# Optimization experiments

Measured on AMD Instinct MI355X. Metric: run time of the kernel, lower is better.

The kernel has to match this reference:

```python
import jax, jax.numpy as jnp
import numpy as np

M, K, N = 8192, 4096, 4096  # tokens, in_features, out_features


def setup_inputs() -> dict:
    key = jax.random.key(0)
    k1, k2, k3, k4, k5, k6 = jax.random.split(key, 6)
    return {
        "x_q": jax.random.randint(k1, (M, K), 0, 256, dtype=jnp.int32),
        "weight_int8": jax.random.randint(k2, (N, K), 0, 256, dtype=jnp.int32),
        "weight_scale": jax.random.uniform(k3, (N, 1), dtype=jnp.float32) * 0.01 + 1e-4,
        "weight_zero_point": jax.random.randint(k4, (N, 1), 0, 256, dtype=jnp.int32),
        "bias": jax.random.normal(k5, (N,), dtype=jnp.float32),
        "input_scale": jax.random.uniform(k6, (1,), dtype=jnp.float32) * 0.05 + 1e-4,
        "input_zero_point": 128,
    }


def reference(x_q, weight_int8, weight_scale, weight_zero_point, bias, input_scale, input_zero_point):
    # zero-point-subtracted fp32 operands (simulated int32 accumulation in fp32)
    x_f = x_q.astype(jnp.float32) - jnp.float32(input_zero_point)      # [M, K]
    w_f = weight_int8.astype(jnp.float32) - weight_zero_point.astype(jnp.float32)  # [N, K]
    acc = jnp.einsum('mk,nk->mn', x_f, w_f)                            # [M, N]
    dequant_scale = input_scale * weight_scale.T                       # [1, N]
    return acc * dequant_scale + bias                                  # [M, N]
```

## Files before the change

### kernel.cpp

```cpp
#include <hip/hip_runtime.h>
#include <hip/hip_bf16.h>
#include <stdint.h>

typedef int v4i __attribute__((ext_vector_type(4)));

#define AS_GLOBAL(p) ((const __attribute__((address_space(1))) void*)(p))
#define AS_LDS(p)    ((__attribute__((address_space(3))) void*)(p))

__global__ __launch_bounds__(256) void prep_kernel(const int* __restrict__ x,
                                                   const int* __restrict__ w,
                                                   const int* __restrict__ izp_p,
                                                   signed char* __restrict__ xs,
                                                   signed char* __restrict__ wsq,
                                                   int* __restrict__ rowsum, int M, int K) {
    int row = blockIdx.x;
    int n4 = K >> 2;
    if (row < M) {
        int izp = izp_p[0];
        const int4* xr = (const int4*)(x + (long)row * K);
        uint32_t* xo = (uint32_t*)(xs + (long)row * K);
        int sum = 0;
        for (int i = threadIdx.x; i < n4; i += 256) {
            int4 v = xr[i];
            int a0 = v.x - izp, a1 = v.y - izp, a2 = v.z - izp, a3 = v.w - izp;
            sum += a0 + a1 + a2 + a3;
            xo[i] = (uint32_t)(a0 & 0xFF) | ((uint32_t)(a1 & 0xFF) << 8) |
                    ((uint32_t)(a2 & 0xFF) << 16) | ((uint32_t)(a3 & 0xFF) << 24);
        }
        sum += __shfl_down(sum, 32);
        sum += __shfl_down(sum, 16);
        sum += __shfl_down(sum, 8);
        sum += __shfl_down(sum, 4);
        sum += __shfl_down(sum, 2);
        sum += __shfl_down(sum, 1);
        __shared__ int red[4];
        if ((threadIdx.x & 63) == 0) red[threadIdx.x >> 6] = sum;
        __syncthreads();
        if (threadIdx.x == 0) rowsum[row] = red[0] + red[1] + red[2] + red[3];
    } else {
        int wrow = row - M;
        const int4* wr = (const int4*)(w + (long)wrow * K);
        uint32_t* wo = (uint32_t*)(wsq + (long)wrow * K);
        for (int i = threadIdx.x; i < n4; i += 256) {
            int4 v = wr[i];
            int a0 = v.x - 128, a1 = v.y - 128, a2 = v.z - 128, a3 = v.w - 128;
            wo[i] = (uint32_t)(a0 & 0xFF) | ((uint32_t)(a1 & 0xFF) << 8) |
                    ((uint32_t)(a2 & 0xFF) << 16) | ((uint32_t)(a3 & 0xFF) << 24);
        }
    }
}


#define BAR  __builtin_amdgcn_s_barrier()
#define LGKM0 asm volatile("s_waitcnt lgkmcnt(0)" ::: "memory")
#define VM8  asm volatile("s_waitcnt vmcnt(8)" ::: "memory")
#define VM0  asm volatile("s_waitcnt vmcnt(0)" ::: "memory")
#define PRIO1 __builtin_amdgcn_s_setprio(1)
#define PRIO0 __builtin_amdgcn_s_setprio(0)

#define STAGE(bb, tile) do {                                                          \
    int t_ = (tile); if (t_ >= NT) t_ = NT - 1;                                       \
    long ko_ = (long)t_ * 64;                                                         \
    signed char* lb_ = lds + (bb) * 32768 + w * 2048;                                 \
    __builtin_amdgcn_global_load_lds(AS_GLOBAL(gA0 + ko_), AS_LDS(lb_),         16, 0, 0); \
    __builtin_amdgcn_global_load_lds(AS_GLOBAL(gA1 + ko_), AS_LDS(lb_ + 1024),  16, 0, 0); \
    __builtin_amdgcn_global_load_lds(AS_GLOBAL(gB0 + ko_), AS_LDS(lb_ + 16384), 16, 0, 0); \
    __builtin_amdgcn_global_load_lds(AS_GLOBAL(gB1 + ko_), AS_LDS(lb_ + 17408), 16, 0, 0); \
  } while (0)

#define M1(mi, ni)                                                                     \
    acc[mi][ni] = __builtin_amdgcn_mfma_i32_16x16x64_i8(af[mi], bf[ni], acc[mi][ni], 0, 0, 0);

__global__ __launch_bounds__(512, 2) void gemm_i8_p4(
    const signed char* __restrict__ A,
    const signed char* __restrict__ B,
    const int* __restrict__ rowsum, const float* __restrict__ wscale,
    const int* __restrict__ wzp, const float* __restrict__ bias,
    const float* __restrict__ iscale, float* __restrict__ C,
    int M, int N, int K) {
  __shared__ signed char lds[131072];
  const int tid = threadIdx.x;
  const int w = tid >> 6, l = tid & 63;
  const int wm = w >> 2, wn = w & 3;
  const int fr = l & 15, fq = l >> 4;

  int nwg = gridDim.x, bid = blockIdx.x;
  if ((nwg & 7) == 0) { int cpx = nwg >> 3; bid = (bid & 7) * cpx + (bid >> 3); }
  const int ntiles = N >> 8;
  const int mt = bid / ntiles, nt = bid - mt * ntiles;
  const long brow = (long)mt << 8, bcol = (long)nt << 8;

  const int NT = K >> 6;

  const int sr = l >> 2;
  const int schunk = ((l & 3) ^ ((l >> 3) & 3)) << 4;
  const signed char* gA0 = A + (brow + (w * 2 + 0) * 16 + sr) * (long)K + schunk;
  const signed char* gA1 = A + (brow + (w * 2 + 1) * 16 + sr) * (long)K + schunk;
  const signed char* gB0 = B + (bcol + (w * 2 + 0) * 16 + sr) * (long)K + schunk;
  const signed char* gB1 = B + (bcol + (w * 2 + 1) * 16 + sr) * (long)K + schunk;

  const int rdc = (fq ^ ((fr >> 1) & 3)) << 4;
  const int aoffc = (wm * 128 + fr) * 64 + rdc;
  const int boffc = 16384 + (wn * 64 + fr) * 64 + rdc;

  v4i acc[8][4] = {};
  v4i af[8], bf[4];

  STAGE(0, 0); STAGE(1, 1); STAGE(2, 2);
  VM8; BAR;

  for (int t = 0; t < NT; ++t) {
    const int bufo = (t & 3) << 15;
#pragma unroll
    for (int mi = 0; mi < 8; ++mi) af[mi] = *(const v4i*)(lds + bufo + aoffc + mi * 1024);
#pragma unroll
    for (int ni = 0; ni < 4; ++ni) bf[ni] = *(const v4i*)(lds + bufo + boffc + ni * 1024);
    STAGE((t + 3) & 3, t + 3);
    PRIO1;
    M1(0, 0) M1(0, 1) M1(0, 2) M1(0, 3)
    M1(1, 0) M1(1, 1) M1(1, 2) M1(1, 3)
    M1(2, 0) M1(2, 1) M1(2, 2) M1(2, 3)
    M1(3, 0) M1(3, 1) M1(3, 2) M1(3, 3)
    M1(4, 0) M1(4, 1) M1(4, 2) M1(4, 3)
    M1(5, 0) M1(5, 1) M1(5, 2) M1(5, 3)
    M1(6, 0) M1(6, 1) M1(6, 2) M1(6, 3)
    M1(7, 0) M1(7, 1) M1(7, 2) M1(7, 3)
    PRIO0;
    LGKM0;
    VM8;
    BAR;
  }

  const float is = iscale[0];
  int rs[8][4];
#pragma unroll
  for (int mi = 0; mi < 8; ++mi)
#pragma unroll
    for (int j = 0; j < 4; ++j)
      rs[mi][j] = rowsum[(int)brow + wm * 128 + mi * 16 + fq * 4 + j];
#pragma unroll
  for (int ni = 0; ni < 4; ++ni) {
    const int col = (int)bcol + wn * 64 + ni * 16 + fr;
    const float sc = is * wscale[col];
    const int zpc = 128 - wzp[col];
    const float bi = bias[col];
#pragma unroll
    for (int mi = 0; mi < 8; ++mi) {
      const int row0 = (int)brow + wm * 128 + mi * 16 + fq * 4;
#pragma unroll
      for (int j = 0; j < 4; ++j) {
        const int v = acc[mi][ni][j] + zpc * rs[mi][j];
        C[(long)(row0 + j) * N + col] = (float)v * sc + bi;
      }
    }
  }
}

extern "C" void kernel_launch(void* const* d_in, const int* in_sizes, int n_in,
                              void* d_out, int out_size, void* d_ws, size_t ws_size,
                              hipStream_t stream) {
    const int* x_q = (const int*)d_in[0];
    const int* w_q = (const int*)d_in[1];
    const float* wscale = (const float*)d_in[2];
    const int* wzp = (const int*)d_in[3];
    const float* bias = (const float*)d_in[4];
    const float* iscale = (const float*)d_in[5];
    const int* izp = (const int*)d_in[6];

    int N = in_sizes[2];
    int K = in_sizes[1] / N;
    int M = in_sizes[0] / K;

    signed char* xs = (signed char*)d_ws;
    signed char* wsq = xs + (size_t)M * K;
    int* rowsum = (int*)(wsq + (size_t)N * K);

    prep_kernel<<<M + N, 256, 0, stream>>>(x_q, w_q, izp, xs, wsq, rowsum, M, K);

    int grid = (M / 256) * (N / 256);
    gemm_i8_p4<<<grid, 512, 0, stream>>>(xs, wsq, rowsum, wscale, wzp, bias, iscale,
                                         (float*)d_out, M, N, K);
}
```

Measured before the change: 192.0 us.

## Load B fragments directly to registers and shrink A LDS staging to double buffer

B operand fragments are now loaded from global memory straight into registers with register double-buffering, while only A is staged through LDS using two 16KB buffers instead of a four-deep 128KB ring. This cuts LDS footprint so more workgroups can reside per CU and removes LDS writes/reads for B. In exchange, the pipeline depth drops to one tile ahead with a full vmcnt(0) wait each iteration, and B global reads are duplicated across waves sharing columns and less coalesced.

Result: slower. 262.9 us (+36.9%).

```diff
diff --git a/kernel.cpp b/kernel.cpp
--- a/kernel.cpp
+++ b/kernel.cpp
@@ -53,32 +53,59 @@
 
 #define BAR  __builtin_amdgcn_s_barrier()
 #define LGKM0 asm volatile("s_waitcnt lgkmcnt(0)" ::: "memory")
-#define VM8  asm volatile("s_waitcnt vmcnt(8)" ::: "memory")
 #define VM0  asm volatile("s_waitcnt vmcnt(0)" ::: "memory")
 #define PRIO1 __builtin_amdgcn_s_setprio(1)
 #define PRIO0 __builtin_amdgcn_s_setprio(0)
 
-#define STAGE(bb, tile) do {                                                          \
-    int t_ = (tile); if (t_ >= NT) t_ = NT - 1;                                       \
-    long ko_ = (long)t_ * 64;                                                         \
-    signed char* lb_ = lds + (bb) * 32768 + w * 2048;                                 \
-    __builtin_amdgcn_global_load_lds(AS_GLOBAL(gA0 + ko_), AS_LDS(lb_),         16, 0, 0); \
-    __builtin_amdgcn_global_load_lds(AS_GLOBAL(gA1 + ko_), AS_LDS(lb_ + 1024),  16, 0, 0); \
-    __builtin_amdgcn_global_load_lds(AS_GLOBAL(gB0 + ko_), AS_LDS(lb_ + 16384), 16, 0, 0); \
-    __builtin_amdgcn_global_load_lds(AS_GLOBAL(gB1 + ko_), AS_LDS(lb_ + 17408), 16, 0, 0); \
+#define STAGE_A(bb, tile) do {                                                        \
+    long ko_ = (long)(tile) * 64;                                                     \
+    signed char* lb_ = lds + (bb) * 16384 + w * 2048;                                 \
+    __builtin_amdgcn_global_load_lds(AS_GLOBAL(gA0 + ko_), AS_LDS(lb_),        16, 0, 0); \
+    __builtin_amdgcn_global_load_lds(AS_GLOBAL(gA1 + ko_), AS_LDS(lb_ + 1024), 16, 0, 0); \
   } while (0)
 
-#define M1(mi, ni)                                                                     \
-    acc[mi][ni] = __builtin_amdgcn_mfma_i32_16x16x64_i8(af[mi], bf[ni], acc[mi][ni], 0, 0, 0);
-
-__global__ __launch_bounds__(512, 2) void gemm_i8_p4(
+#define M1(mi, ni, BC)                                                                 \
+    acc[mi][ni] = __builtin_amdgcn_mfma_i32_16x16x64_i8(af[mi], BC[ni], acc[mi][ni], 0, 0, 0);
+
+#define MFMA32(BC) do {                                                                \
+    M1(0, 0, BC) M1(0, 1, BC) M1(0, 2, BC) M1(0, 3, BC)                                \
+    M1(1, 0, BC) M1(1, 1, BC) M1(1, 2, BC) M1(1, 3, BC)                                \
+    M1(2, 0, BC) M1(2, 1, BC) M1(2, 2, BC) M1(2, 3, BC)                                \
+    M1(3, 0, BC) M1(3, 1, BC) M1(3, 2, BC) M1(3, 3, BC)                                \
+    M1(4, 0, BC) M1(4, 1, BC) M1(4, 2, BC) M1(4, 3, BC)                                \
+    M1(5, 0, BC) M1(5, 1, BC) M1(5, 2, BC) M1(5, 3, BC)                                \
+    M1(6, 0, BC) M1(6, 1, BC) M1(6, 2, BC) M1(6, 3, BC)                                \
+    M1(7, 0, BC) M1(7, 1, BC) M1(7, 2, BC) M1(7, 3, BC)                                \
+  } while (0)
+
+#define ITER(b, BC, BN, t) do {                                                        \
+    int tn_ = (t) + 1; if (tn_ >= NT) tn_ = NT - 1;                                    \
+    long bo_ = (long)tn_ * 64;                                                         \
+    BN[0] = *(const v4i*)(gBf0 + bo_);                                                 \
+    BN[1] = *(const v4i*)(gBf1 + bo_);                                                 \
+    BN[2] = *(const v4i*)(gBf2 + bo_);                                                 \
+    BN[3] = *(const v4i*)(gBf3 + bo_);                                                 \
+    STAGE_A((b) ^ 1, tn_);                                                             \
+    af[0] = *(const v4i*)(lds + (b) * 16384 + aoffc + 0 * 1024);                       \
+    af[1] = *(const v4i*)(lds + (b) * 16384 + aoffc + 1 * 1024);                       \
+    af[2] = *(const v4i*)(lds + (b) * 16384 + aoffc + 2 * 1024);                       \
+    af[3] = *(const v4i*)(lds + (b) * 16384 + aoffc + 3 * 1024);                       \
+    af[4] = *(const v4i*)(lds + (b) * 16384 + aoffc + 4 * 1024);                       \
+    af[5] = *(const v4i*)(lds + (b) * 16384 + aoffc + 5 * 1024);                       \
+    af[6] = *(const v4i*)(lds + (b) * 16384 + aoffc + 6 * 1024);                       \
+    af[7] = *(const v4i*)(lds + (b) * 16384 + aoffc + 7 * 1024);                       \
+    PRIO1; MFMA32(BC); PRIO0;                                                          \
+    LGKM0; VM0; BAR;                                                                   \
+  } while (0)
+
+__global__ __launch_bounds__(512, 2) void gemm_i8_bd(
     const signed char* __restrict__ A,
     const signed char* __restrict__ B,
     const int* __restrict__ rowsum, const float* __restrict__ wscale,
     const int* __restrict__ wzp, const float* __restrict__ bias,
     const float* __restrict__ iscale, float* __restrict__ C,
     int M, int N, int K) {
-  __shared__ signed char lds[131072];
+  __shared__ signed char lds[32768];
   const int tid = threadIdx.x;
   const int w = tid >> 6, l = tid & 63;
   const int wm = w >> 2, wn = w & 3;
@@ -96,39 +123,29 @@
   const int schunk = ((l & 3) ^ ((l >> 3) & 3)) << 4;
   const signed char* gA0 = A + (brow + (w * 2 + 0) * 16 + sr) * (long)K + schunk;
   const signed char* gA1 = A + (brow + (w * 2 + 1) * 16 + sr) * (long)K + schunk;
-  const signed char* gB0 = B + (bcol + (w * 2 + 0) * 16 + sr) * (long)K + schunk;
-  const signed char* gB1 = B + (bcol + (w * 2 + 1) * 16 + sr) * (long)K + schunk;
 
   const int rdc = (fq ^ ((fr >> 1) & 3)) << 4;
   const int aoffc = (wm * 128 + fr) * 64 + rdc;
-  const int boffc = 16384 + (wn * 64 + fr) * 64 + rdc;
+
+  const signed char* gBf0 = B + (bcol + wn * 64 + 0 * 16 + fr) * (long)K + fq * 16;
+  const signed char* gBf1 = B + (bcol + wn * 64 + 1 * 16 + fr) * (long)K + fq * 16;
+  const signed char* gBf2 = B + (bcol + wn * 64 + 2 * 16 + fr) * (long)K + fq * 16;
+  const signed char* gBf3 = B + (bcol + wn * 64 + 3 * 16 + fr) * (long)K + fq * 16;
 
   v4i acc[8][4] = {};
-  v4i af[8], bf[4];
-
-  STAGE(0, 0); STAGE(1, 1); STAGE(2, 2);
-  VM8; BAR;
-
-  for (int t = 0; t < NT; ++t) {
-    const int bufo = (t & 3) << 15;
-#pragma unroll
-    for (int mi = 0; mi < 8; ++mi) af[mi] = *(const v4i*)(lds + bufo + aoffc + mi * 1024);
-#pragma unroll
-    for (int ni = 0; ni < 4; ++ni) bf[ni] = *(const v4i*)(lds + bufo + boffc + ni * 1024);
-    STAGE((t + 3) & 3, t + 3);
-    PRIO1;
-    M1(0, 0) M1(0, 1) M1(0, 2) M1(0, 3)
-    M1(1, 0) M1(1, 1) M1(1, 2) M1(1, 3)
-    M1(2, 0) M1(2, 1) M1(2, 2) M1(2, 3)
-    M1(3, 0) M1(3, 1) M1(3, 2) M1(3, 3)
-    M1(4, 0) M1(4, 1) M1(4, 2) M1(4, 3)
-    M1(5, 0) M1(5, 1) M1(5, 2) M1(5, 3)
-    M1(6, 0) M1(6, 1) M1(6, 2) M1(6, 3)
-    M1(7, 0) M1(7, 1) M1(7, 2) M1(7, 3)
-    PRIO0;
-    LGKM0;
-    VM8;
-    BAR;
+  v4i af[8];
+  v4i bfA[4], bfB[4];
+
+  STAGE_A(0, 0);
+  bfA[0] = *(const v4i*)(gBf0);
+  bfA[1] = *(const v4i*)(gBf1);
+  bfA[2] = *(const v4i*)(gBf2);
+  bfA[3] = *(const v4i*)(gBf3);
+  VM0; BAR;
+
+  for (int t = 0; t < NT; t += 2) {
+    ITER(0, bfA, bfB, t);
+    ITER(1, bfB, bfA, t + 1);
   }
 
   const float is = iscale[0];
@@ -178,6 +195,6 @@
     prep_kernel<<<M + N, 256, 0, stream>>>(x_q, w_q, izp, xs, wsq, rowsum, M, K);
 
     int grid = (M / 256) * (N / 256);
-    gemm_i8_p4<<<grid, 512, 0, stream>>>(xs, wsq, rowsum, wscale, wzp, bias, iscale,
+    gemm_i8_bd<<<grid, 512, 0, stream>>>(xs, wsq, rowsum, wscale, wzp, bias, iscale,
                                          (float*)d_out, M, N, K);
 }
```
